# Optimization experiments

Hardware: AMD Instinct MI355X
Metric: run time of the kernel (lower is better)

The kernel has to match this reference:

```python
import jax, jax.numpy as jnp
import numpy as np

B, TL, TG, K, H = 32, 4096, 1, 128, 8


def setup_inputs() -> dict:
    key = jax.random.key(0)
    ks = jax.random.split(key, 7)
    return {
        "x_local": jax.random.normal(ks[0], (B, TL, K), jnp.float32),
        "x_glob": jax.random.normal(ks[1], (B, TG, K), jnp.float32),
        # weights stored (in_features, out_features) so y = x @ W, matching torch Linear math
        "Wq": jax.random.normal(ks[2], (K, K * H), jnp.float32) / np.sqrt(K).astype(np.float32),
        "Wk": jax.random.normal(ks[3], (K, K * H), jnp.float32) / np.sqrt(K).astype(np.float32),
        "Wv": jax.random.normal(ks[4], (K, K * H), jnp.float32) / np.sqrt(K).astype(np.float32),
        "Wu": jax.random.normal(ks[5], (H * K, K), jnp.float32) / np.sqrt(H * K).astype(np.float32),
        "bu": jnp.zeros((K,), jnp.float32),
    }


def reference(x_local, x_glob, Wq, Wk, Wv, Wu, bu):
    b, t_l, k = x_local.shape
    t_g = x_glob.shape[1]
    h = Wq.shape[1] // k
    scale = k ** -0.25  # applied to both q and k, as in the original

    # projections -> (b, h, t, k)
    q = (x_glob @ Wq).reshape(b, t_g, h, k).transpose(0, 2, 1, 3) * scale
    kk = (x_local @ Wk).reshape(b, t_l, h, k).transpose(0, 2, 1, 3) * scale
    v = (x_local @ Wv).reshape(b, t_l, h, k).transpose(0, 2, 1, 3)

    # dot = bmm(q, k^T).transpose(1,2) -> (b, h, t_l, t_g)
    dot = jnp.einsum('bhgk,bhlk->bhlg', q, kk)
    # softmax over t_l (dim=1 of the (bh, t_l, t_g) tensor in torch)
    attn = jax.nn.softmax(dot, axis=2)  # dropout rate 0 -> identity

    # elementwise mul (t_g==1 broadcasts against k) then sum over t_l
    out = attn * v                                  # (b, h, t_l, k)
    out = out.transpose(0, 2, 1, 3).reshape(b, t_l, h * k)
    out = out.sum(axis=1)                           # (b, h*k)
    return out @ Wu + bu                            # (b, k)
```

## Files before the change

### kernel.cpp

```cpp
#include <hip/hip_runtime.h>

#define BB 32
#define TL 4096
#define KK 128
#define HH 8
#define SCALE2 0.08838834764831845f

#define NCHB 16
#define NCHC 16

#define OFF_WK  0
#define N_WK    (BB*HH*KK)
#define OFF_P   (OFF_WK + N_WK)
#define N_P     (BB*TL*HH)
#define OFF_DEN (OFF_P + N_P)
#define N_DEN   (BB*HH*NCHB)
#define OFF_XA  (OFF_DEN + N_DEN)
#define N_XA    (BB*NCHC*HH*KK)

__global__ __launch_bounds__(128) void sa_kA(
    const float* __restrict__ xg, const float* __restrict__ Wq,
    const float* __restrict__ Wk, float* __restrict__ wk_eff) {
  int bh = blockIdx.x;
  int b = bh >> 3, h = bh & 7;
  int t = threadIdx.x;
  __shared__ float xgs[KK];
  __shared__ float qh[KK];
  xgs[t] = xg[b * KK + t];
  __syncthreads();
  float acc = 0.f;
  const float* wq = Wq + h * KK + t;
  for (int c2 = 0; c2 < KK; ++c2) acc += xgs[c2] * wq[c2 * (HH * KK)];
  qh[t] = acc;
  __syncthreads();
  const float4* wk4 = (const float4*)(Wk + t * (HH * KK) + h * KK);
  const float4* qh4 = (const float4*)qh;
  float acc2 = 0.f;
  #pragma unroll 8
  for (int c4 = 0; c4 < KK / 4; ++c4) {
    float4 a = wk4[c4];
    float4 q4 = qh4[c4];
    acc2 += a.x * q4.x + a.y * q4.y + a.z * q4.z + a.w * q4.w;
  }
  wk_eff[bh * KK + t] = acc2 * SCALE2;
}

__global__ __launch_bounds__(512) void sa_kB(
    const float* __restrict__ x, const float* __restrict__ wk_eff,
    float* __restrict__ pbuf, float* __restrict__ denP) {
  const int chunk = blockIdx.x;
  const int b = blockIdx.y;
  const int t = threadIdx.x;
  const int lane16 = t & 15;
  const int g = t >> 4;
  float wkr[HH][8];
  const float* wkb = wk_eff + (b * HH) * KK + lane16 * 8;
  #pragma unroll
  for (int h = 0; h < HH; ++h) {
    float4 a = *(const float4*)(wkb + h * KK);
    float4 c = *(const float4*)(wkb + h * KK + 4);
    wkr[h][0] = a.x; wkr[h][1] = a.y; wkr[h][2] = a.z; wkr[h][3] = a.w;
    wkr[h][4] = c.x; wkr[h][5] = c.y; wkr[h][6] = c.z; wkr[h][7] = c.w;
  }
  float den = 0.f;
  const int rows = TL / NCHB;
  const int l0 = chunk * rows;
  for (int i = 0; i < rows / 32; ++i) {
    int l = l0 + g + i * 32;
    const float* xr = x + ((size_t)b * TL + l) * KK + lane16 * 8;
    float4 xa = *(const float4*)xr;
    float4 xb = *(const float4*)(xr + 4);
    float part[HH];
    #pragma unroll
    for (int h = 0; h < HH; ++h) {
      part[h] = xa.x * wkr[h][0] + xa.y * wkr[h][1] + xa.z * wkr[h][2] + xa.w * wkr[h][3]
              + xb.x * wkr[h][4] + xb.y * wkr[h][5] + xb.z * wkr[h][6] + xb.w * wkr[h][7];
    }
    #pragma unroll
    for (int s = 1; s < 16; s <<= 1) {
      #pragma unroll
      for (int h = 0; h < HH; ++h) part[h] += __shfl_xor(part[h], s, 64);
    }
    if (lane16 < 8) {
      float d = part[0];
      #pragma unroll
      for (int h = 1; h < HH; ++h) d = (lane16 == h) ? part[h] : d;
      float p = __expf(d);
      pbuf[((size_t)b * TL + l) * HH + lane16] = p;
      den += p;
    }
  }
  __shared__ float denl[32][8];
  if (lane16 < 8) denl[g][lane16] = den;
  __syncthreads();
  if (t < 8) {
    float s = 0.f;
    for (int gg = 0; gg < 32; ++gg) s += denl[gg][t];
    denP[(b * HH + t) * NCHB + chunk] = s;
  }
}

__global__ __launch_bounds__(512) void sa_kC(
    const float* __restrict__ x, const float* __restrict__ pbuf,
    float* __restrict__ xattnP) {
  const int chunk = blockIdx.x;
  const int b = blockIdx.y;
  const int t = threadIdx.x;
  const int c4 = t & 31;
  const int rg = t >> 5;
  float acc[HH][4];
  #pragma unroll
  for (int h = 0; h < HH; ++h) {
    acc[h][0] = 0.f; acc[h][1] = 0.f; acc[h][2] = 0.f; acc[h][3] = 0.f;
  }
  const int rows = TL / NCHC;
  const int l0 = chunk * rows;
  for (int i = 0; i < rows / 16; ++i) {
    int l = l0 + rg + i * 16;
    float4 xv = *(const float4*)(x + ((size_t)b * TL + l) * KK + c4 * 4);
    float4 pa = *(const float4*)(pbuf + ((size_t)b * TL + l) * HH);
    float4 pb = *(const float4*)(pbuf + ((size_t)b * TL + l) * HH + 4);
    float pv[8] = {pa.x, pa.y, pa.z, pa.w, pb.x, pb.y, pb.z, pb.w};
    #pragma unroll
    for (int h = 0; h < HH; ++h) {
      acc[h][0] += pv[h] * xv.x;
      acc[h][1] += pv[h] * xv.y;
      acc[h][2] += pv[h] * xv.z;
      acc[h][3] += pv[h] * xv.w;
    }
  }
  __shared__ float red[8][HH * KK];
  if (rg >= 8) {
    #pragma unroll
    for (int h = 0; h < HH; ++h)
      *(float4*)&red[rg - 8][h * KK + c4 * 4] = make_float4(acc[h][0], acc[h][1], acc[h][2], acc[h][3]);
  }
  __syncthreads();
  if (rg < 8) {
    #pragma unroll
    for (int h = 0; h < HH; ++h) {
      float4* dst = (float4*)&red[rg][h * KK + c4 * 4];
      float4 o = *dst;
      o.x += acc[h][0]; o.y += acc[h][1]; o.z += acc[h][2]; o.w += acc[h][3];
      *dst = o;
    }
  }
  __syncthreads();
  #pragma unroll
  for (int s = 4; s >= 1; s >>= 1) {
    if (rg < s) {
      #pragma unroll
      for (int h = 0; h < HH; ++h) {
        float4* dst = (float4*)&red[rg][h * KK + c4 * 4];
        float4 o = *(float4*)&red[rg + s][h * KK + c4 * 4];
        float4 d0 = *dst;
        d0.x += o.x; d0.y += o.y; d0.z += o.z; d0.w += o.w;
        *dst = d0;
      }
    }
    __syncthreads();
  }
  const int base = (b * NCHC + chunk) * (HH * KK);
  for (int v = t; v < HH * KK; v += 512) xattnP[base + v] = red[0][v];
}

__global__ __launch_bounds__(128) void sa_kD(
    const float* __restrict__ xattnP, const float* __restrict__ denP,
    const float* __restrict__ Wv, const float* __restrict__ Wu,
    const float* __restrict__ bu, float* __restrict__ out) {
  const int bh = blockIdx.x;
  const int b = bh >> 3, h = bh & 7;
  const int t = threadIdx.x;
  float den = 0.f;
  #pragma unroll
  for (int cb = 0; cb < NCHB; ++cb) den += denP[(b * HH + h) * NCHB + cb];
  float acc = 0.f;
  #pragma unroll
  for (int ch = 0; ch < NCHC; ++ch)
    acc += xattnP[(b * NCHC + ch) * (HH * KK) + h * KK + t];
  __shared__ float u[KK];
  u[t] = acc / den;
  __syncthreads();
  float sk = 0.f;
  const float* wv = Wv + h * KK + t;
  for (int c = 0; c < KK; ++c) sk += u[c] * wv[c * (HH * KK)];
  __shared__ float sl[KK];
  sl[t] = sk;
  __syncthreads();
  float po = (h == 0) ? bu[t] : 0.f;
  const float* wu = Wu + (h * KK) * KK + t;
  for (int k = 0; k < KK; ++k) po += sl[k] * wu[k * KK];
  atomicAdd(&out[b * KK + t], po);
}

extern "C" void kernel_launch(void* const* d_in, const int* in_sizes, int n_in,
                              void* d_out, int out_size, void* d_ws, size_t ws_size,
                              hipStream_t stream) {
  const float* x  = (const float*)d_in[0];
  const float* xg = (const float*)d_in[1];
  const float* Wq = (const float*)d_in[2];
  const float* Wk = (const float*)d_in[3];
  const float* Wv = (const float*)d_in[4];
  const float* Wu = (const float*)d_in[5];
  const float* bu = (const float*)d_in[6];
  float* out = (float*)d_out;

  float* ws     = (float*)d_ws;
  float* wk_eff = ws + OFF_WK;
  float* pbuf   = ws + OFF_P;
  float* denP   = ws + OFF_DEN;
  float* xattnP = ws + OFF_XA;

  hipMemsetAsync(d_out, 0, (size_t)out_size * sizeof(float), stream);
  sa_kA<<<dim3(BB * HH), dim3(128), 0, stream>>>(xg, Wq, Wk, wk_eff);
  sa_kB<<<dim3(NCHB, BB), dim3(512), 0, stream>>>(x, wk_eff, pbuf, denP);
  sa_kC<<<dim3(NCHC, BB), dim3(512), 0, stream>>>(x, pbuf, xattnP);
  sa_kD<<<dim3(BB * HH), dim3(128), 0, stream>>>(xattnP, denP, Wv, Wu, bu, out);
}
```

Baseline: 56.00 us.

## Fuse score and weighted-sum passes into one kernel; fuse final projection per batch

Merges the exp-score kernel and the attention-weighted accumulation kernel so x_local is read once and the per-row probability buffer is no longer written to and read back from memory. Each thread accumulates unnormalized exp-weighted sums for all heads in registers, reduced with shuffles and shared memory. The final projection becomes one block per batch without atomics, which removes the output memset. The costs are a grid of only 256 blocks and heavy register pressure from 64 accumulators plus 64 weights, which may lower occupancy.

After: 61.52 us. 1.1x slower.

```diff
diff --git a/kernel.cpp b/kernel.cpp
--- a/kernel.cpp
+++ b/kernel.cpp
@@ -6,17 +6,14 @@
 #define HH 8
 #define SCALE2 0.08838834764831845f
 
-#define NCHB 16
-#define NCHC 16
+#define NCH 8
 
 #define OFF_WK  0
 #define N_WK    (BB*HH*KK)
-#define OFF_P   (OFF_WK + N_WK)
-#define N_P     (BB*TL*HH)
-#define OFF_DEN (OFF_P + N_P)
-#define N_DEN   (BB*HH*NCHB)
-#define OFF_XA  (OFF_DEN + N_DEN)
-#define N_XA    (BB*NCHC*HH*KK)
+#define OFF_XA  (OFF_WK + N_WK)
+#define N_XA    (BB*NCH*HH*KK)
+#define OFF_DEN (OFF_XA + N_XA)
+#define N_DEN   (BB*NCH*HH)
 
 __global__ __launch_bounds__(128) void sa_kA(
     const float* __restrict__ xg, const float* __restrict__ Wq,
@@ -45,14 +42,15 @@
   wk_eff[bh * KK + t] = acc2 * SCALE2;
 }
 
-__global__ __launch_bounds__(512) void sa_kB(
+__global__ __launch_bounds__(512) void sa_kF(
     const float* __restrict__ x, const float* __restrict__ wk_eff,
-    float* __restrict__ pbuf, float* __restrict__ denP) {
+    float* __restrict__ xattnP, float* __restrict__ denP) {
   const int chunk = blockIdx.x;
   const int b = blockIdx.y;
   const int t = threadIdx.x;
   const int lane16 = t & 15;
   const int g = t >> 4;
+
   float wkr[HH][8];
   const float* wkb = wk_eff + (b * HH) * KK + lane16 * 8;
   #pragma unroll
@@ -62,12 +60,21 @@
     wkr[h][0] = a.x; wkr[h][1] = a.y; wkr[h][2] = a.z; wkr[h][3] = a.w;
     wkr[h][4] = c.x; wkr[h][5] = c.y; wkr[h][6] = c.z; wkr[h][7] = c.w;
   }
-  float den = 0.f;
-  const int rows = TL / NCHB;
+  float acc[HH][8];
+  float den[HH];
+  #pragma unroll
+  for (int h = 0; h < HH; ++h) {
+    den[h] = 0.f;
+    #pragma unroll
+    for (int j = 0; j < 8; ++j) acc[h][j] = 0.f;
+  }
+
+  const int rows = TL / NCH;
   const int l0 = chunk * rows;
+  #pragma unroll 2
   for (int i = 0; i < rows / 32; ++i) {
-    int l = l0 + g + i * 32;
-    const float* xr = x + ((size_t)b * TL + l) * KK + lane16 * 8;
+    const int l = l0 + i * 32 + g;
+    const float* xr = x + ((size_t)(b * TL + l)) * KK + lane16 * 8;
     float4 xa = *(const float4*)xr;
     float4 xb = *(const float4*)(xr + 4);
     float part[HH];
@@ -81,116 +88,99 @@
       #pragma unroll
       for (int h = 0; h < HH; ++h) part[h] += __shfl_xor(part[h], s, 64);
     }
-    if (lane16 < 8) {
-      float d = part[0];
-      #pragma unroll
-      for (int h = 1; h < HH; ++h) d = (lane16 == h) ? part[h] : d;
-      float p = __expf(d);
-      pbuf[((size_t)b * TL + l) * HH + lane16] = p;
-      den += p;
-    }
-  }
-  __shared__ float denl[32][8];
-  if (lane16 < 8) denl[g][lane16] = den;
-  __syncthreads();
-  if (t < 8) {
-    float s = 0.f;
-    for (int gg = 0; gg < 32; ++gg) s += denl[gg][t];
-    denP[(b * HH + t) * NCHB + chunk] = s;
-  }
-}
-
-__global__ __launch_bounds__(512) void sa_kC(
-    const float* __restrict__ x, const float* __restrict__ pbuf,
-    float* __restrict__ xattnP) {
-  const int chunk = blockIdx.x;
-  const int b = blockIdx.y;
-  const int t = threadIdx.x;
-  const int c4 = t & 31;
-  const int rg = t >> 5;
-  float acc[HH][4];
+    #pragma unroll
+    for (int h = 0; h < HH; ++h) {
+      float p = __expf(part[h]);
+      den[h] += p;
+      acc[h][0] += p * xa.x; acc[h][1] += p * xa.y;
+      acc[h][2] += p * xa.z; acc[h][3] += p * xa.w;
+      acc[h][4] += p * xb.x; acc[h][5] += p * xb.y;
+      acc[h][6] += p * xb.z; acc[h][7] += p * xb.w;
+    }
+  }
+
   #pragma unroll
   for (int h = 0; h < HH; ++h) {
-    acc[h][0] = 0.f; acc[h][1] = 0.f; acc[h][2] = 0.f; acc[h][3] = 0.f;
-  }
-  const int rows = TL / NCHC;
-  const int l0 = chunk * rows;
-  for (int i = 0; i < rows / 16; ++i) {
-    int l = l0 + rg + i * 16;
-    float4 xv = *(const float4*)(x + ((size_t)b * TL + l) * KK + c4 * 4);
-    float4 pa = *(const float4*)(pbuf + ((size_t)b * TL + l) * HH);
-    float4 pb = *(const float4*)(pbuf + ((size_t)b * TL + l) * HH + 4);
-    float pv[8] = {pa.x, pa.y, pa.z, pa.w, pb.x, pb.y, pb.z, pb.w};
-    #pragma unroll
-    for (int h = 0; h < HH; ++h) {
-      acc[h][0] += pv[h] * xv.x;
-      acc[h][1] += pv[h] * xv.y;
-      acc[h][2] += pv[h] * xv.z;
-      acc[h][3] += pv[h] * xv.w;
-    }
-  }
+    #pragma unroll
+    for (int j = 0; j < 8; ++j) {
+      acc[h][j] += __shfl_xor(acc[h][j], 16, 64);
+      acc[h][j] += __shfl_xor(acc[h][j], 32, 64);
+    }
+    den[h] += __shfl_xor(den[h], 16, 64);
+    den[h] += __shfl_xor(den[h], 32, 64);
+  }
+
   __shared__ float red[8][HH * KK];
-  if (rg >= 8) {
+  __shared__ float redD[8][HH];
+  const int wv = t >> 6, ln = t & 63;
+  if (ln < 16) {
     #pragma unroll
     for (int h = 0; h < HH; ++h)
-      *(float4*)&red[rg - 8][h * KK + c4 * 4] = make_float4(acc[h][0], acc[h][1], acc[h][2], acc[h][3]);
-  }
-  __syncthreads();
-  if (rg < 8) {
-    #pragma unroll
-    for (int h = 0; h < HH; ++h) {
-      float4* dst = (float4*)&red[rg][h * KK + c4 * 4];
-      float4 o = *dst;
-      o.x += acc[h][0]; o.y += acc[h][1]; o.z += acc[h][2]; o.w += acc[h][3];
-      *dst = o;
-    }
-  }
-  __syncthreads();
-  #pragma unroll
-  for (int s = 4; s >= 1; s >>= 1) {
-    if (rg < s) {
       #pragma unroll
-      for (int h = 0; h < HH; ++h) {
-        float4* dst = (float4*)&red[rg][h * KK + c4 * 4];
-        float4 o = *(float4*)&red[rg + s][h * KK + c4 * 4];
-        float4 d0 = *dst;
-        d0.x += o.x; d0.y += o.y; d0.z += o.z; d0.w += o.w;
-        *dst = d0;
-      }
-    }
-    __syncthreads();
-  }
-  const int base = (b * NCHC + chunk) * (HH * KK);
-  for (int v = t; v < HH * KK; v += 512) xattnP[base + v] = red[0][v];
-}
-
-__global__ __launch_bounds__(128) void sa_kD(
+      for (int j = 0; j < 8; ++j)
+        red[wv][h * KK + ln * 8 + j] = acc[h][j];
+    if (ln < HH) redD[wv][ln] = den[ln];
+  }
+  __syncthreads();
+  const size_t base = ((size_t)(b * NCH + chunk)) * (HH * KK);
+  for (int e = t; e < HH * KK; e += 512) {
+    float s = 0.f;
+    #pragma unroll
+    for (int w = 0; w < 8; ++w) s += red[w][e];
+    xattnP[base + e] = s;
+  }
+  if (t < HH) {
+    float s = 0.f;
+    #pragma unroll
+    for (int w = 0; w < 8; ++w) s += redD[w][t];
+    denP[(b * NCH + chunk) * HH + t] = s;
+  }
+}
+
+__global__ __launch_bounds__(512) void sa_kE(
     const float* __restrict__ xattnP, const float* __restrict__ denP,
     const float* __restrict__ Wv, const float* __restrict__ Wu,
     const float* __restrict__ bu, float* __restrict__ out) {
-  const int bh = blockIdx.x;
-  const int b = bh >> 3, h = bh & 7;
+  const int b = blockIdx.x;
   const int t = threadIdx.x;
-  float den = 0.f;
-  #pragma unroll
-  for (int cb = 0; cb < NCHB; ++cb) den += denP[(b * HH + h) * NCHB + cb];
-  float acc = 0.f;
-  #pragma unroll
-  for (int ch = 0; ch < NCHC; ++ch)
-    acc += xattnP[(b * NCHC + ch) * (HH * KK) + h * KK + t];
-  __shared__ float u[KK];
-  u[t] = acc / den;
-  __syncthreads();
-  float sk = 0.f;
-  const float* wv = Wv + h * KK + t;
-  for (int c = 0; c < KK; ++c) sk += u[c] * wv[c * (HH * KK)];
-  __shared__ float sl[KK];
-  sl[t] = sk;
-  __syncthreads();
-  float po = (h == 0) ? bu[t] : 0.f;
-  const float* wu = Wu + (h * KK) * KK + t;
-  for (int k = 0; k < KK; ++k) po += sl[k] * wu[k * KK];
-  atomicAdd(&out[b * KK + t], po);
+  __shared__ float uS[HH][KK + 1];
+  __shared__ float sS[HH * KK];
+  __shared__ float dS[HH];
+  __shared__ float oS[4][KK];
+
+  if (t < HH) {
+    float d = 0.f;
+    #pragma unroll
+    for (int ch = 0; ch < NCH; ++ch) d += denP[(b * NCH + ch) * HH + t];
+    dS[t] = d;
+  }
+  __syncthreads();
+  for (int e = t; e < HH * KK; e += 512) {
+    float a = 0.f;
+    #pragma unroll
+    for (int ch = 0; ch < NCH; ++ch)
+      a += xattnP[((size_t)(b * NCH + ch)) * (HH * KK) + e];
+    uS[e >> 7][e & 127] = a / dS[e >> 7];
+  }
+  __syncthreads();
+  for (int e = t; e < HH * KK; e += 512) {
+    const int h = e >> 7;
+    const float* wv = Wv + e;
+    const float* uh = uS[h];
+    float sv = 0.f;
+    #pragma unroll 8
+    for (int c = 0; c < KK; ++c) sv += uh[c] * wv[(size_t)c * (HH * KK)];
+    sS[e] = sv;
+  }
+  __syncthreads();
+  const int cp = t & 127, q = t >> 7;
+  float po = 0.f;
+  const float* wu = Wu + cp;
+  #pragma unroll 8
+  for (int k = q * 256; k < (q + 1) * 256; ++k) po += sS[k] * wu[(size_t)k * KK];
+  oS[q][cp] = po;
+  __syncthreads();
+  if (t < KK) out[b * KK + t] = oS[0][t] + oS[1][t] + oS[2][t] + oS[3][t] + bu[t];
 }
 
 extern "C" void kernel_launch(void* const* d_in, const int* in_sizes, int n_in,
@@ -207,13 +197,10 @@
 
   float* ws     = (float*)d_ws;
   float* wk_eff = ws + OFF_WK;
-  float* pbuf   = ws + OFF_P;
+  float* xattnP = ws + OFF_XA;
   float* denP   = ws + OFF_DEN;
-  float* xattnP = ws + OFF_XA;
-
-  hipMemsetAsync(d_out, 0, (size_t)out_size * sizeof(float), stream);
+
   sa_kA<<<dim3(BB * HH), dim3(128), 0, stream>>>(xg, Wq, Wk, wk_eff);
-  sa_kB<<<dim3(NCHB, BB), dim3(512), 0, stream>>>(x, wk_eff, pbuf, denP);
-  sa_kC<<<dim3(NCHC, BB), dim3(512), 0, stream>>>(x, pbuf, xattnP);
-  sa_kD<<<dim3(BB * HH), dim3(128), 0, stream>>>(xattnP, denP, Wv, Wu, bu, out);
-}
+  sa_kF<<<dim3(NCH, BB), dim3(512), 0, stream>>>(x, wk_eff, xattnP, denP);
+  sa_kE<<<dim3(BB), dim3(512), 0, stream>>>(xattnP, denP, Wv, Wu, bu, out);
+}
```
